# Performance work log

Measured on AMD Instinct MI355X. Metric: run time of the kernel, lower is better.

The kernel has to match this reference:

```python
import jax, jax.numpy as jnp
import numpy as np
from jax.scipy.special import logsumexp

B, S, T = 64, 2048, 256


def setup_inputs() -> dict:
    key = jax.random.key(0)
    k1, k2, k3, k4, k5 = jax.random.split(key, 5)
    emissions = jax.random.normal(k1, (B, S, T), dtype=jnp.float32)
    tags = jax.random.randint(k2, (B, S), 0, T, dtype=jnp.int32)
    mask = jnp.ones((B, S), dtype=jnp.int32)
    transitions = jax.random.uniform(k3, (T, T), jnp.float32, -0.1, 0.1)
    start_transitions = jax.random.uniform(k4, (T,), jnp.float32, -0.1, 0.1)
    end_transitions = jax.random.uniform(k5, (T,), jnp.float32, -0.1, 0.1)
    return {
        "emissions": emissions,
        "tags": tags,
        "mask": mask,
        "transitions": transitions,
        "start_transitions": start_transitions,
        "end_transitions": end_transitions,
    }


def reference(emissions, tags, mask, transitions, start_transitions, end_transitions):
    # batch-first layout: emissions [B,S,T], tags/mask [B,S]
    b, s, t = emissions.shape
    m = mask.astype(emissions.dtype)
    batch_idx = jnp.arange(b)

    # ---- numerator: score of the gold tag sequence ----
    # emission score at every position: [B,S]
    emit_sc = jnp.take_along_axis(emissions, tags[:, :, None], axis=2)[:, :, 0]
    score = start_transitions[tags[:, 0]] + emit_sc[:, 0]
    # NOTE: original indexes transitions[cur_tag, prev_tag] here (kept faithful)
    trans_sc = transitions[tags[:, 1:], tags[:, :-1]]
    score = score + jnp.sum((trans_sc + emit_sc[:, 1:]) * m[:, 1:], axis=1)
    seq_ends = mask.sum(axis=1) - 1  # [B]
    last_tags = tags[batch_idx, seq_ends]
    score = score + end_transitions[last_tags]

    # ---- denominator: log partition via forward algorithm (mask is a no-op
    # in the original normalizer, kept faithful) ----
    alpha0 = start_transitions + emissions[:, 0]  # [B,T]

    def step(alpha, emit_t):
        # scores[b,i,j] = alpha[b,i] + transitions[i,j]; logsumexp over prev tag i
        alpha = logsumexp(alpha[:, :, None] + transitions[None, :, :], axis=1) + emit_t
        return alpha, None

    emissions_t = jnp.swapaxes(emissions, 0, 1)[1:]  # [S-1, B, T]
    alpha, _ = jax.lax.scan(step, alpha0, emissions_t)
    log_z = logsumexp(alpha + end_transitions, axis=1)  # [B]

    llh = score - log_z
    return llh.mean()  # reduction='mean'
```

## Files before the change

kernel.cpp:

```cpp
#include <hip/hip_runtime.h>
#include <hip/hip_bf16.h>

#define B_ 64
#define S_ 2048
#define T_ 256

typedef __attribute__((ext_vector_type(8))) short bf16x8;
typedef __attribute__((ext_vector_type(4))) float f32x4;

template <int CTRL>
__device__ __forceinline__ float dpp_max(float v) {
  const int t = __builtin_amdgcn_update_dpp(0, __builtin_bit_cast(int, v), CTRL, 0xF, 0xF, true);
  return fmaxf(v, __builtin_bit_cast(float, t));
}
template <int CTRL>
__device__ __forceinline__ float dpp_add(float v) {
  const int t = __builtin_amdgcn_update_dpp(0, __builtin_bit_cast(int, v), CTRL, 0xF, 0xF, true);
  return v + __builtin_bit_cast(float, t);
}

__device__ __forceinline__ unsigned short f2bf(float f) {
  unsigned u = __builtin_bit_cast(unsigned, f);
  u += 0x7FFFu + ((u >> 16) & 1u);
  return (unsigned short)(u >> 16);
}

__device__ __forceinline__ f32x4 mfma16(bf16x8 a, bf16x8 b, f32x4 c) {
  return __builtin_amdgcn_mfma_f32_16x16x32_bf16(a, b, c, 0, 0, 0);
}

__device__ __forceinline__ void wg_barrier() {
  __builtin_amdgcn_sched_barrier(0);
  asm volatile("s_waitcnt lgkmcnt(0)" ::: "memory");
  __builtin_amdgcn_s_barrier();
  asm volatile("" ::: "memory");
  __builtin_amdgcn_sched_barrier(0);
}

__global__ void crf_score(const float* __restrict__ em, const int* __restrict__ tags,
                          const int* __restrict__ mask, const float* __restrict__ trans,
                          const float* __restrict__ startt, const float* __restrict__ endt,
                          float* __restrict__ ws) {
  const int b = blockIdx.x;
  const int t = threadIdx.x;
  const int* tg = tags + b * S_;
  const int* mk = mask + b * S_;
  const float* eb = em + (size_t)b * S_ * T_;

  float sc = 0.f;
  int msum = 0;
  for (int s = t; s < S_; s += 256) {
    const int tag = tg[s];
    const int m = mk[s];
    msum += m;
    const float e = eb[(size_t)s * T_ + tag];
    if (s == 0) {
      sc += startt[tag] + e;
    } else {
      const int pt = tg[s - 1];
      sc += (trans[tag * T_ + pt] + e) * (float)m;
    }
  }
#pragma unroll
  for (int off = 32; off > 0; off >>= 1) {
    sc += __shfl_down(sc, off);
    msum += __shfl_down(msum, off);
  }
  __shared__ float ssc[4];
  __shared__ int smc[4];
  const int wv = t >> 6, ln = t & 63;
  if (ln == 0) { ssc[wv] = sc; smc[wv] = msum; }
  __syncthreads();
  if (t == 0) {
    const float s4 = (ssc[0] + ssc[1]) + (ssc[2] + ssc[3]);
    const int m4 = smc[0] + smc[1] + smc[2] + smc[3];
    const int last = tg[m4 - 1];
    ws[b] = s4 + endt[last];
  }
}

#define STEP(RB, WB, P)                                                           \
  {                                                                               \
    const float4 q = ((const float4*)&mpT[RB][0])[l & 3];                         \
    float mh = fmaxf(fmaxf(q.x, q.y), fmaxf(q.z, q.w));                           \
    mh = dpp_max<0xB1>(mh);                                                       \
    mh = dpp_max<0x4E>(mh);                                                       \
    int ue = (int)(__builtin_bit_cast(unsigned, mh) >> 23) - 127;                 \
    ue = (ue < -20) ? -20 : ue;                                                   \
    ue += 8;                                                                      \
    k_run += ue;                                                                  \
    const float kln = -0.6931471805599453f * (float)ue;                           \
    const float EcRs = __expf(P + kln);                                           \
    P = emL[cOff + rowf];                                                         \
    rowf = (rowf < 2047u * 256u) ? rowf + 256u : rowf;                            \
    const unsigned char* xb = &Xl[RB][0];                                         \
    f32x4 z4 = {0.f, 0.f, 0.f, 0.f};                                              \
    f32x4 aL0 = z4, aL1 = z4, aL2 = z4, aL3 = z4;                                 \
    f32x4 aH0 = z4, aH1 = z4, aH2 = z4, aH3 = z4;                                 \
    _Pragma("unroll") for (int kk = 0; kk < 4; ++kk) {                            \
      const bf16x8 av = *(const bf16x8*)(xb + raddr[kk]);                         \
      aL0 = mfma16(av, wf[0][kk], aL0);                                           \
      aL1 = mfma16(av, wf[1][kk], aL1);                                           \
      aL2 = mfma16(av, wf[2][kk], aL2);                                           \
      aL3 = mfma16(av, wf[3][kk], aL3);                                           \
    }                                                                             \
    _Pragma("unroll") for (int kk = 4; kk < 8; ++kk) {                            \
      const bf16x8 av = *(const bf16x8*)(xb + raddr[kk]);                         \
      aH0 = mfma16(av, wf[0][kk], aH0);                                           \
      aH1 = mfma16(av, wf[1][kk], aH1);                                           \
      aH2 = mfma16(av, wf[2][kk], aH2);                                           \
      aH3 = mfma16(av, wf[3][kk], aH3);                                           \
    }                                                                             \
    const float c0 = aL0[0] + aH0[0], c1 = aL1[0] + aH1[0];                       \
    const float c2 = aL2[0] + aH2[0], c3 = aL3[0] + aH3[0];                       \
    const float s01 = (hi & 1) ? c1 : c0;                                         \
    const float s23 = (hi & 1) ? c3 : c2;                                         \
    const float val = (hi & 2) ? s23 : s01;                                       \
    const float xfb = val * EcRs;                                                 \
    float mx = xfb;                                                               \
    mx = dpp_max<0xB1>(mx);                                                       \
    mx = dpp_max<0x4E>(mx);                                                       \
    mx = dpp_max<0x141>(mx);                                                      \
    mx = dpp_max<0x140>(mx);                                                      \
    if (lo == 0) mpT[WB][w * 4 + hi] = mx;                                        \
    *(unsigned short*)(&Xl[WB][0] + waddr) = f2bf(xfb);                           \
    wg_barrier();                                                                 \
  }

__global__ __launch_bounds__(256, 1) void crf_forward(
    const float* __restrict__ em, const float* __restrict__ trans,
    const float* __restrict__ startt, const float* __restrict__ endt,
    float* __restrict__ ws) {
  const int tid = threadIdx.x;
  const int w = tid >> 6;
  const int l = tid & 63;
  const int lo = l & 15;
  const int hi = l >> 4;

  __shared__ __align__(16) unsigned char Xl[2][512];
  __shared__ __align__(16) float mpT[2][16];
  __shared__ float fsum[4];

  bf16x8 wf[4][8];
#pragma unroll
  for (int t = 0; t < 4; ++t) {
    const int j = 64 * w + 16 * t + lo;
#pragma unroll
    for (int kk = 0; kk < 8; ++kk) {
      bf16x8 v;
#pragma unroll
      for (int e = 0; e < 8; ++e) {
        const int k = kk * 32 + hi * 8 + e;
        v[e] = (short)f2bf(__expf(trans[k * T_ + j]));
      }
      wf[t][kk] = v;
    }
  }

  unsigned raddr[8];
#pragma unroll
  for (int kk = 0; kk < 8; ++kk) raddr[kk] = (unsigned)(16 * ((4 * kk + hi) & 31));
  const int jE = 64 * w + 16 * hi + lo;
  const unsigned waddr = (unsigned)(16 * ((jE >> 3) & 31) + (jE & 7) * 2);
  const float* emL = em + jE;
  const unsigned cOff = (unsigned)(blockIdx.x * (S_ * T_));

  float m0;
  {
    const float al = startt[jE] + emL[cOff];
    float lm = al;
    lm = dpp_max<0xB1>(lm);
    lm = dpp_max<0x4E>(lm);
    lm = dpp_max<0x141>(lm);
    lm = dpp_max<0x140>(lm);
    lm = fmaxf(lm, __shfl_xor(lm, 16));
    lm = fmaxf(lm, __shfl_xor(lm, 32));
    if (l == 0) fsum[w] = lm;
    __syncthreads();
    m0 = fmaxf(fmaxf(fsum[0], fsum[1]), fmaxf(fsum[2], fsum[3]));
    const float x0 = __expf(al - m0);
    *(unsigned short*)(&Xl[0][0] + waddr) = f2bf(x0);
    if (tid < 16) mpT[0][tid] = 1.0f;
  }
  float P0 = emL[cOff + 256];
  float P1 = emL[cOff + 512];
  unsigned rowf = 3u * 256u;
  int k_run = 0;
  __syncthreads();

  for (int p2 = 0; p2 < (S_ - 2) / 2; ++p2) {
    STEP(0, 1, P0)
    STEP(1, 0, P1)
  }

  float xtail;
  {
    const float4 q = ((const float4*)&mpT[0][0])[l & 3];
    float mh = fmaxf(fmaxf(q.x, q.y), fmaxf(q.z, q.w));
    mh = dpp_max<0xB1>(mh);
    mh = dpp_max<0x4E>(mh);
    int ue = (int)(__builtin_bit_cast(unsigned, mh) >> 23) - 127;
    ue = (ue < -20) ? -20 : ue;
    ue += 8;
    k_run += ue;
    const float kln = -0.6931471805599453f * (float)ue;
    const float EcRs = __expf(P0 + kln);
    const unsigned char* xb = &Xl[0][0];
    f32x4 z4 = {0.f, 0.f, 0.f, 0.f};
    f32x4 aL0 = z4, aL1 = z4, aL2 = z4, aL3 = z4;
    f32x4 aH0 = z4, aH1 = z4, aH2 = z4, aH3 = z4;
#pragma unroll
    for (int kk = 0; kk < 4; ++kk) {
      const bf16x8 av = *(const bf16x8*)(xb + raddr[kk]);
      aL0 = mfma16(av, wf[0][kk], aL0);
      aL1 = mfma16(av, wf[1][kk], aL1);
      aL2 = mfma16(av, wf[2][kk], aL2);
      aL3 = mfma16(av, wf[3][kk], aL3);
    }
#pragma unroll
    for (int kk = 4; kk < 8; ++kk) {
      const bf16x8 av = *(const bf16x8*)(xb + raddr[kk]);
      aH0 = mfma16(av, wf[0][kk], aH0);
      aH1 = mfma16(av, wf[1][kk], aH1);
      aH2 = mfma16(av, wf[2][kk], aH2);
      aH3 = mfma16(av, wf[3][kk], aH3);
    }
    const float c0 = aL0[0] + aH0[0], c1 = aL1[0] + aH1[0];
    const float c2 = aL2[0] + aH2[0], c3 = aL3[0] + aH3[0];
    const float s01 = (hi & 1) ? c1 : c0;
    const float s23 = (hi & 1) ? c3 : c2;
    const float val = (hi & 2) ? s23 : s01;
    xtail = val * EcRs;
  }

  float f = xtail * __expf(endt[jE]);
  f = dpp_add<0xB1>(f);
  f = dpp_add<0x4E>(f);
  f = dpp_add<0x141>(f);
  f = dpp_add<0x140>(f);
  f += __shfl_xor(f, 16);
  f += __shfl_xor(f, 32);
  __syncthreads();
  if (l == 0) fsum[w] = f;
  __syncthreads();
  if (tid == 0) {
    const float tot = (fsum[0] + fsum[1]) + (fsum[2] + fsum[3]);
    ws[64 + blockIdx.x] = m0 + (float)k_run * 0.6931471805599453f + __logf(tot);
  }
}

__global__ void crf_final(const float* __restrict__ ws, float* __restrict__ out) {
  const int t = threadIdx.x;
  float v = ws[t] - ws[64 + t];
#pragma unroll
  for (int off = 1; off <= 32; off <<= 1) v += __shfl_xor(v, off);
  if (t == 0) out[0] = v * (1.0f / 64.0f);
}

extern "C" void kernel_launch(void* const* d_in, const int* in_sizes, int n_in,
                              void* d_out, int out_size, void* d_ws, size_t ws_size,
                              hipStream_t stream) {
  const float* em = (const float*)d_in[0];
  const int* tags = (const int*)d_in[1];
  const int* mask = (const int*)d_in[2];
  const float* trans = (const float*)d_in[3];
  const float* startt = (const float*)d_in[4];
  const float* endt = (const float*)d_in[5];
  float* out = (float*)d_out;
  float* ws = (float*)d_ws;

  crf_score<<<B_, 256, 0, stream>>>(em, tags, mask, trans, startt, endt, ws);
  crf_forward<<<B_, 256, 0, stream>>>(em, trans, startt, endt, ws);
  crf_final<<<1, 64, 0, stream>>>(ws, out);
}
```

Baseline: 973.9 us.

## Split per-step matvec between MFMA and packed fp16 dot products

Each wave now computes half of its 64 output tags with f16 MFMA (two tiles instead of four) and the other half with v_dot2 fp16 dot products on the VALU, followed by cross-lane shuffles. The aim is to shorten the serial MFMA dependency chain in each recurrence step by running matrix and vector units in parallel. Storage switches from bf16 to fp16, which gains mantissa precision but narrows dynamic range. It also adds extra emission loads, exps and shuffles per step, and holds more weights in registers.

```diff
diff --git a/kernel.cpp b/kernel.cpp
--- a/kernel.cpp
+++ b/kernel.cpp
@@ -5,9 +5,17 @@
 #define S_ 2048
 #define T_ 256
 
-typedef __attribute__((ext_vector_type(8))) short bf16x8;
+typedef _Float16 half2_t __attribute__((ext_vector_type(2)));
+typedef _Float16 f16x8 __attribute__((ext_vector_type(8)));
 typedef __attribute__((ext_vector_type(4))) float f32x4;
-
+typedef __attribute__((ext_vector_type(4))) unsigned u32x4;
+
+__device__ __forceinline__ float fdot2f(half2_t a, half2_t b, float c) {
+  return __builtin_amdgcn_fdot2(a, b, c, false);
+}
+__device__ __forceinline__ half2_t pack2(float a, float b) {
+  return __builtin_bit_cast(half2_t, __builtin_amdgcn_cvt_pkrtz(a, b));
+}
 template <int CTRL>
 __device__ __forceinline__ float dpp_max(float v) {
   const int t = __builtin_amdgcn_update_dpp(0, __builtin_bit_cast(int, v), CTRL, 0xF, 0xF, true);
@@ -19,14 +27,8 @@
   return v + __builtin_bit_cast(float, t);
 }
 
-__device__ __forceinline__ unsigned short f2bf(float f) {
-  unsigned u = __builtin_bit_cast(unsigned, f);
-  u += 0x7FFFu + ((u >> 16) & 1u);
-  return (unsigned short)(u >> 16);
-}
-
-__device__ __forceinline__ f32x4 mfma16(bf16x8 a, bf16x8 b, f32x4 c) {
-  return __builtin_amdgcn_mfma_f32_16x16x32_bf16(a, b, c, 0, 0, 0);
+__device__ __forceinline__ f32x4 mfma16h(f16x8 a, f16x8 b, f32x4 c) {
+  return __builtin_amdgcn_mfma_f32_16x16x32_f16(a, b, c, 0, 0, 0);
 }
 
 __device__ __forceinline__ void wg_barrier() {
@@ -79,9 +81,44 @@
   }
 }
 
-#define STEP(RB, WB, P)                                                           \
+#define STEP(RB, WB, P, PV1, PV2)                                                 \
   {                                                                               \
     const float4 q = ((const float4*)&mpT[RB][0])[l & 3];                         \
+    const unsigned char* xb = &Xl[RB][0];                                         \
+    f16x8 av[8];                                                                  \
+    _Pragma("unroll") for (int kk = 0; kk < 8; ++kk)                              \
+      av[kk] = *(const f16x8*)(xb + raddr[kk]);                                   \
+    f32x4 z4 = {0.f, 0.f, 0.f, 0.f};                                              \
+    f32x4 aL0 = z4, aH0 = z4, aL1 = z4, aH1 = z4;                                 \
+    _Pragma("unroll") for (int kk = 0; kk < 4; ++kk) {                            \
+      aL0 = mfma16h(av[kk], wf[0][kk], aL0);                                      \
+      aL1 = mfma16h(av[kk], wf[1][kk], aL1);                                      \
+    }                                                                             \
+    _Pragma("unroll") for (int kk = 4; kk < 8; ++kk) {                            \
+      aH0 = mfma16h(av[kk], wf[0][kk], aH0);                                      \
+      aH1 = mfma16h(av[kk], wf[1][kk], aH1);                                      \
+    }                                                                             \
+    float v1a = 0.f, v1b = 0.f, v1c = 0.f, v1d = 0.f;                             \
+    float v2a = 0.f, v2b = 0.f, v2c = 0.f, v2d = 0.f;                             \
+    _Pragma("unroll") for (int kk = 0; kk < 8; ++kk) {                            \
+      const u32x4 u = __builtin_bit_cast(u32x4, av[kk]);                          \
+      const half2_t h0 = __builtin_bit_cast(half2_t, u.x);                        \
+      const half2_t h1 = __builtin_bit_cast(half2_t, u.y);                        \
+      const half2_t h2 = __builtin_bit_cast(half2_t, u.z);                        \
+      const half2_t h3 = __builtin_bit_cast(half2_t, u.w);                        \
+      v1a = fdot2f(h0, Wd1[kk][0], v1a);                                          \
+      v1b = fdot2f(h1, Wd1[kk][1], v1b);                                          \
+      v1c = fdot2f(h2, Wd1[kk][2], v1c);                                          \
+      v1d = fdot2f(h3, Wd1[kk][3], v1d);                                          \
+      v2a = fdot2f(h0, Wd2[kk][0], v2a);                                          \
+      v2b = fdot2f(h1, Wd2[kk][1], v2b);                                          \
+      v2c = fdot2f(h2, Wd2[kk][2], v2c);                                          \
+      v2d = fdot2f(h3, Wd2[kk][3], v2d);                                          \
+    }                                                                             \
+    float zv1 = (v1a + v1b) + (v1c + v1d);                                        \
+    float zv2 = (v2a + v2b) + (v2c + v2d);                                        \
+    zv1 += __shfl_xor(zv1, 16); zv1 += __shfl_xor(zv1, 32);                       \
+    zv2 += __shfl_xor(zv2, 16); zv2 += __shfl_xor(zv2, 32);                       \
     float mh = fmaxf(fmaxf(q.x, q.y), fmaxf(q.z, q.w));                           \
     mh = dpp_max<0xB1>(mh);                                                       \
     mh = dpp_max<0x4E>(mh);                                                       \
@@ -91,39 +128,25 @@
     k_run += ue;                                                                  \
     const float kln = -0.6931471805599453f * (float)ue;                           \
     const float EcRs = __expf(P + kln);                                           \
+    const float EcRsV1 = __expf(PV1 + kln);                                       \
+    const float EcRsV2 = __expf(PV2 + kln);                                       \
     P = emL[cOff + rowf];                                                         \
+    PV1 = emV1[cOff + rowf];                                                      \
+    PV2 = emV2[cOff + rowf];                                                      \
     rowf = (rowf < 2047u * 256u) ? rowf + 256u : rowf;                            \
-    const unsigned char* xb = &Xl[RB][0];                                         \
-    f32x4 z4 = {0.f, 0.f, 0.f, 0.f};                                              \
-    f32x4 aL0 = z4, aL1 = z4, aL2 = z4, aL3 = z4;                                 \
-    f32x4 aH0 = z4, aH1 = z4, aH2 = z4, aH3 = z4;                                 \
-    _Pragma("unroll") for (int kk = 0; kk < 4; ++kk) {                            \
-      const bf16x8 av = *(const bf16x8*)(xb + raddr[kk]);                         \
-      aL0 = mfma16(av, wf[0][kk], aL0);                                           \
-      aL1 = mfma16(av, wf[1][kk], aL1);                                           \
-      aL2 = mfma16(av, wf[2][kk], aL2);                                           \
-      aL3 = mfma16(av, wf[3][kk], aL3);                                           \
-    }                                                                             \
-    _Pragma("unroll") for (int kk = 4; kk < 8; ++kk) {                            \
-      const bf16x8 av = *(const bf16x8*)(xb + raddr[kk]);                         \
-      aH0 = mfma16(av, wf[0][kk], aH0);                                           \
-      aH1 = mfma16(av, wf[1][kk], aH1);                                           \
-      aH2 = mfma16(av, wf[2][kk], aH2);                                           \
-      aH3 = mfma16(av, wf[3][kk], aH3);                                           \
-    }                                                                             \
-    const float c0 = aL0[0] + aH0[0], c1 = aL1[0] + aH1[0];                       \
-    const float c2 = aL2[0] + aH2[0], c3 = aL3[0] + aH3[0];                       \
-    const float s01 = (hi & 1) ? c1 : c0;                                         \
-    const float s23 = (hi & 1) ? c3 : c2;                                         \
-    const float val = (hi & 2) ? s23 : s01;                                       \
-    const float xfb = val * EcRs;                                                 \
-    float mx = xfb;                                                               \
+    const f32x4 ac0 = aL0 + aH0, ac1 = aL1 + aH1;                                 \
+    const float valm = (hi & 1) ? ac1[0] : ac0[0];                                \
+    const float xm = valm * EcRs;                                                 \
+    const float xv1 = zv1 * EcRsV1;                                               \
+    const float xv2 = zv2 * EcRsV2;                                               \
+    const float own = (hi < 2) ? xm : ((hi == 2) ? xv1 : xv2);                    \
+    float mx = fmaxf(own, fmaxf(xv1, xv2));                                       \
     mx = dpp_max<0xB1>(mx);                                                       \
     mx = dpp_max<0x4E>(mx);                                                       \
     mx = dpp_max<0x141>(mx);                                                      \
     mx = dpp_max<0x140>(mx);                                                      \
     if (lo == 0) mpT[WB][w * 4 + hi] = mx;                                        \
-    *(unsigned short*)(&Xl[WB][0] + waddr) = f2bf(xfb);                           \
+    *(_Float16*)(&Xl[WB][0] + waddr) = (_Float16)own;                             \
     wg_barrier();                                                                 \
   }
 
@@ -141,20 +164,33 @@
   __shared__ __align__(16) float mpT[2][16];
   __shared__ float fsum[4];
 
-  bf16x8 wf[4][8];
-#pragma unroll
-  for (int t = 0; t < 4; ++t) {
+  f16x8 wf[2][4 + 4];
+#pragma unroll
+  for (int t = 0; t < 2; ++t) {
     const int j = 64 * w + 16 * t + lo;
 #pragma unroll
     for (int kk = 0; kk < 8; ++kk) {
-      bf16x8 v;
+      f16x8 v;
 #pragma unroll
       for (int e = 0; e < 8; ++e) {
         const int k = kk * 32 + hi * 8 + e;
-        v[e] = (short)f2bf(__expf(trans[k * T_ + j]));
+        v[e] = (_Float16)__expf(trans[k * T_ + j]);
       }
       wf[t][kk] = v;
     }
+  }
+  half2_t Wd1[8][4], Wd2[8][4];
+  {
+    const int j1 = 64 * w + 32 + lo;
+    const int j2 = 64 * w + 48 + lo;
+#pragma unroll
+    for (int kk = 0; kk < 8; ++kk)
+#pragma unroll
+      for (int p = 0; p < 4; ++p) {
+        const int k0 = kk * 32 + hi * 8 + 2 * p;
+        Wd1[kk][p] = pack2(__expf(trans[k0 * T_ + j1]), __expf(trans[(k0 + 1) * T_ + j1]));
+        Wd2[kk][p] = pack2(__expf(trans[k0 * T_ + j2]), __expf(trans[(k0 + 1) * T_ + j2]));
+      }
   }
 
   unsigned raddr[8];
@@ -163,6 +199,8 @@
   const int jE = 64 * w + 16 * hi + lo;
   const unsigned waddr = (unsigned)(16 * ((jE >> 3) & 31) + (jE & 7) * 2);
   const float* emL = em + jE;
+  const float* emV1 = em + 64 * w + 32 + lo;
+  const float* emV2 = em + 64 * w + 48 + lo;
   const unsigned cOff = (unsigned)(blockIdx.x * (S_ * T_));
 
   float m0;
@@ -179,23 +217,62 @@
     __syncthreads();
     m0 = fmaxf(fmaxf(fsum[0], fsum[1]), fmaxf(fsum[2], fsum[3]));
     const float x0 = __expf(al - m0);
-    *(unsigned short*)(&Xl[0][0] + waddr) = f2bf(x0);
+    *(_Float16*)(&Xl[0][0] + waddr) = (_Float16)x0;
     if (tid < 16) mpT[0][tid] = 1.0f;
   }
-  float P0 = emL[cOff + 256];
-  float P1 = emL[cOff + 512];
+  float P0 = emL[cOff + 256], P1 = emL[cOff + 512];
+  float PV1a = emV1[cOff + 256], PV1b = emV1[cOff + 512];
+  float PV2a = emV2[cOff + 256], PV2b = emV2[cOff + 512];
   unsigned rowf = 3u * 256u;
   int k_run = 0;
   __syncthreads();
 
   for (int p2 = 0; p2 < (S_ - 2) / 2; ++p2) {
-    STEP(0, 1, P0)
-    STEP(1, 0, P1)
-  }
-
-  float xtail;
+    STEP(0, 1, P0, PV1a, PV2a)
+    STEP(1, 0, P1, PV1b, PV2b)
+  }
+
+  float own;
   {
     const float4 q = ((const float4*)&mpT[0][0])[l & 3];
+    const unsigned char* xb = &Xl[0][0];
+    f16x8 av[8];
+#pragma unroll
+    for (int kk = 0; kk < 8; ++kk) av[kk] = *(const f16x8*)(xb + raddr[kk]);
+    f32x4 z4 = {0.f, 0.f, 0.f, 0.f};
+    f32x4 aL0 = z4, aH0 = z4, aL1 = z4, aH1 = z4;
+#pragma unroll
+    for (int kk = 0; kk < 4; ++kk) {
+      aL0 = mfma16h(av[kk], wf[0][kk], aL0);
+      aL1 = mfma16h(av[kk], wf[1][kk], aL1);
+    }
+#pragma unroll
+    for (int kk = 4; kk < 8; ++kk) {
+      aH0 = mfma16h(av[kk], wf[0][kk], aH0);
+      aH1 = mfma16h(av[kk], wf[1][kk], aH1);
+    }
+    float v1a = 0.f, v1b = 0.f, v1c = 0.f, v1d = 0.f;
+    float v2a = 0.f, v2b = 0.f, v2c = 0.f, v2d = 0.f;
+#pragma unroll
+    for (int kk = 0; kk < 8; ++kk) {
+      const u32x4 u = __builtin_bit_cast(u32x4, av[kk]);
+      const half2_t h0 = __builtin_bit_cast(half2_t, u.x);
+      const half2_t h1 = __builtin_bit_cast(half2_t, u.y);
+      const half2_t h2 = __builtin_bit_cast(half2_t, u.z);
+      const half2_t h3 = __builtin_bit_cast(half2_t, u.w);
+      v1a = fdot2f(h0, Wd1[kk][0], v1a);
+      v1b = fdot2f(h1, Wd1[kk][1], v1b);
+      v1c = fdot2f(h2, Wd1[kk][2], v1c);
+      v1d = fdot2f(h3, Wd1[kk][3], v1d);
+      v2a = fdot2f(h0, Wd2[kk][0], v2a);
+      v2b = fdot2f(h1, Wd2[kk][1], v2b);
+      v2c = fdot2f(h2, Wd2[kk][2], v2c);
+      v2d = fdot2f(h3, Wd2[kk][3], v2d);
+    }
+    float zv1 = (v1a + v1b) + (v1c + v1d);
+    float zv2 = (v2a + v2b) + (v2c + v2d);
+    zv1 += __shfl_xor(zv1, 16); zv1 += __shfl_xor(zv1, 32);
+    zv2 += __shfl_xor(zv2, 16); zv2 += __shfl_xor(zv2, 32);
     float mh = fmaxf(fmaxf(q.x, q.y), fmaxf(q.z, q.w));
     mh = dpp_max<0xB1>(mh);
     mh = dpp_max<0x4E>(mh);
@@ -205,35 +282,17 @@
     k_run += ue;
     const float kln = -0.6931471805599453f * (float)ue;
     const float EcRs = __expf(P0 + kln);
-    const unsigned char* xb = &Xl[0][0];
-    f32x4 z4 = {0.f, 0.f, 0.f, 0.f};
-    f32x4 aL0 = z4, aL1 = z4, aL2 = z4, aL3 = z4;
-    f32x4 aH0 = z4, aH1 = z4, aH2 = z4, aH3 = z4;
-#pragma unroll
-    for (int kk = 0; kk < 4; ++kk) {
-      const bf16x8 av = *(const bf16x8*)(xb + raddr[kk]);
-      aL0 = mfma16(av, wf[0][kk], aL0);
-      aL1 = mfma16(av, wf[1][kk], aL1);
-      aL2 = mfma16(av, wf[2][kk], aL2);
-      aL3 = mfma16(av, wf[3][kk], aL3);
-    }
-#pragma unroll
-    for (int kk = 4; kk < 8; ++kk) {
-      const bf16x8 av = *(const bf16x8*)(xb + raddr[kk]);
-      aH0 = mfma16(av, wf[0][kk], aH0);
-      aH1 = mfma16(av, wf[1][kk], aH1);
-      aH2 = mfma16(av, wf[2][kk], aH2);
-      aH3 = mfma16(av, wf[3][kk], aH3);
-    }
-    const float c0 = aL0[0] + aH0[0], c1 = aL1[0] + aH1[0];
-    const float c2 = aL2[0] + aH2[0], c3 = aL3[0] + aH3[0];
-    const float s01 = (hi & 1) ? c1 : c0;
-    const float s23 = (hi & 1) ? c3 : c2;
-    const float val = (hi & 2) ? s23 : s01;
-    xtail = val * EcRs;
-  }
-
-  float f = xtail * __expf(endt[jE]);
+    const float EcRsV1 = __expf(PV1a + kln);
+    const float EcRsV2 = __expf(PV2a + kln);
+    const f32x4 ac0 = aL0 + aH0, ac1 = aL1 + aH1;
+    const float valm = (hi & 1) ? ac1[0] : ac0[0];
+    const float xm = valm * EcRs;
+    const float xv1 = zv1 * EcRsV1;
+    const float xv2 = zv2 * EcRsV2;
+    own = (hi < 2) ? xm : ((hi == 2) ? xv1 : xv2);
+  }
+
+  float f = own * __expf(endt[jE]);
   f = dpp_add<0xB1>(f);
   f = dpp_add<0x4E>(f);
   f = dpp_add<0x141>(f);
```

Result: slower. 1.257 ms (+29.1%).
